# Kernel tuning notes

Hardware: AMD Instinct MI355X
Metric: run time of the kernel (lower is better)

Reference implementation:

```python
import jax, jax.numpy as jnp
import numpy as np

BS, D_IN, D_H, D_Z = 4096, 784, 400, 20


def setup_inputs() -> dict:
    key = jax.random.key(0)
    ks = jax.random.split(key, 13)
    s = 0.05
    return {
        "x": jax.random.normal(ks[0], (BS, D_IN), dtype=jnp.float32),
        "W1": jax.random.normal(ks[1], (D_H, D_IN), dtype=jnp.float32) * s,
        "b1": jax.random.normal(ks[2], (D_H,), dtype=jnp.float32) * s,
        "W21": jax.random.normal(ks[3], (D_Z, D_H), dtype=jnp.float32) * s,
        "b21": jax.random.normal(ks[4], (D_Z,), dtype=jnp.float32) * s,
        "W22": jax.random.normal(ks[5], (D_Z, D_H), dtype=jnp.float32) * s,
        "b22": jax.random.normal(ks[6], (D_Z,), dtype=jnp.float32) * s,
        "W3": jax.random.normal(ks[7], (D_H, D_Z), dtype=jnp.float32) * s,
        "b3": jax.random.normal(ks[8], (D_H,), dtype=jnp.float32) * s,
        "W41": jax.random.normal(ks[9], (D_IN, D_H), dtype=jnp.float32) * s,
        "b41": jax.random.normal(ks[10], (D_IN,), dtype=jnp.float32) * s,
        "W42": jax.random.normal(ks[11], (D_IN, D_H), dtype=jnp.float32) * s,
        "b42": jax.random.normal(ks[12], (D_IN,), dtype=jnp.float32) * s,
    }


def reference(x, W1, b1, W21, b21, W22, b22, W3, b3, W41, b41, W42, b42):
    xr = x.reshape(-1, D_IN)                              # [bs, 784]
    # encode
    h1 = jax.nn.relu(xr @ W1.T + b1)                      # [bs, 400]
    mu = h1 @ W21.T + b21                                 # [bs, 20]
    logvar = h1 @ W22.T + b22                             # [bs, 20]
    # unscented sigma points: varsqrt[:, i] = sqrt(N)*logvar[:, i]*e_i
    N = D_Z
    sqrtN = jnp.asarray(np.sqrt(N), dtype=x.dtype)
    # delta[i, b, j] = sqrt(N) * logvar[b, i] * (i == j)   -> [N, bs, N]
    delta = sqrtN * logvar.T[:, :, None] * jnp.eye(N, dtype=x.dtype)[:, None, :]
    z = jnp.concatenate([mu[None] + delta, mu[None] - delta], axis=0)  # [2N, bs, N]

    def decode(zs):
        h3 = jax.nn.relu(zs @ W3.T + b3)                  # [bs, 400]
        return zs @ W41.T * 0 + (h3 @ W41.T + b41), h3 @ W42.T + b42

    def decode_clean(zs):
        h3 = jax.nn.relu(zs @ W3.T + b3)
        return h3 @ W41.T + b41, h3 @ W42.T + b42

    # original loop decodes every sigma point; recon_x keeps the last one
    mu_x, var_x = jax.vmap(decode_clean)(z)               # each [2N, bs, 784]
    recon_mu = mu_x[-1]
    recon_var = var_x[-1]
    return recon_mu, recon_var, mu, logvar, z
```

## Files before the change

kernel.cpp:

```cpp
#include <hip/hip_runtime.h>
#include <hip/hip_bf16.h>

#define BS   4096
#define DIN  784
#define DH   400
#define DZ   20

#define KPH  416
#define KPD  448

#define OFF_RMU  0
#define OFF_RVAR 3211264
#define OFF_MU   6422528
#define OFF_LV   6504448
#define OFF_Z    6586368

#define WS_WCAT  0
#define WS_W2C   1404928
#define WS_H1B   1444864
#define WS_H3B   4852736

#define SQRT20F 4.47213595499958f

using short8 = __attribute__((ext_vector_type(8))) short;
using f4     = __attribute__((ext_vector_type(4))) float;

__device__ __forceinline__ short bf16r(float f) {
    union { float f; unsigned u; } v; v.f = f;
    unsigned r = (v.u + 0x7fffu + ((v.u >> 16) & 1u)) >> 16;
    return (short)r;
}

__device__ __forceinline__ void glds16(const void* g, void* l) {
    __builtin_amdgcn_global_load_lds(
        (const __attribute__((address_space(1))) unsigned int*)g,
        (__attribute__((address_space(3))) unsigned int*)l,
        16, 0, 0);
}

__global__ __launch_bounds__(256)
void k1(const float* __restrict__ x, const float* __restrict__ W1,
        const float* __restrict__ b1,
        const float* __restrict__ W41, const float* __restrict__ W42,
        const float* __restrict__ W21, const float* __restrict__ W22,
        short* __restrict__ h1b, char* __restrict__ ws) {
    __shared__ short sA[2][64 * 64];
    __shared__ short sB[2][80 * 64];

    const int tid = threadIdx.x;
    const int bid = blockIdx.x;

    if (bid >= 320) {
        short* wcat = (short*)(ws + WS_WCAT);
        short* w2c  = (short*)(ws + WS_W2C);
        const int NC = 1568 * 56 + 48 * 52;
        for (int p = (bid - 320) * 256 + tid; p < NC; p += 64 * 256) {
            const float* sr = nullptr;
            short* dst;
            int c;
            if (p < 1568 * 56) {
                int row = p / 56; c = p - row * 56;
                sr = (row < 784) ? (W41 + (size_t)row * DH)
                                 : (W42 + (size_t)(row - 784) * DH);
                dst = wcat + (size_t)row * KPD + c * 8;
            } else {
                int q = p - 1568 * 56;
                int row = q / 52; c = q - row * 52;
                if (row < 20)      sr = W21 + (size_t)row * DH;
                else if (row < 40) sr = W22 + (size_t)(row - 20) * DH;
                dst = w2c + (size_t)row * KPH + c * 8;
            }
            short8 v;
            if (c < 50 && sr) {
                f4 a = *(const f4*)(sr + c * 8);
                f4 b = *(const f4*)(sr + c * 8 + 4);
#pragma unroll
                for (int e = 0; e < 4; ++e) { v[e] = bf16r(a[e]); v[4 + e] = bf16r(b[e]); }
            } else {
#pragma unroll
                for (int e = 0; e < 8; ++e) v[e] = 0;
            }
            *(short8*)dst = v;
        }
        return;
    }

    const int swz = (bid & 7) * 40 + (bid >> 3);
    const int bm = swz / 5, bn = swz - bm * 5;
    const int w = tid >> 6, l = tid & 63, lg = l >> 4, lr = l & 15;

    f4 acc[5] = {};
    f4 ar[4];
    f4 br[6];

    auto a_load = [&](int kt) {
#pragma unroll
        for (int i = 0; i < 2; ++i) {
            int c = tid + i * 256;
            int row = c >> 3, kc = c & 7;
            int gk = kt * 64 + kc * 8;
            if (gk < DIN) {
                const float* src = x + (size_t)(bm * 64 + row) * DIN + gk;
                ar[2 * i] = *(const f4*)src;
                ar[2 * i + 1] = *(const f4*)(src + 4);
            } else {
                ar[2 * i] = (f4){0.f, 0.f, 0.f, 0.f};
                ar[2 * i + 1] = (f4){0.f, 0.f, 0.f, 0.f};
            }
        }
    };
    auto b_load = [&](int kt) {
#pragma unroll
        for (int i = 0; i < 3; ++i) {
            int c = tid + i * 256;
            if (c < 640) {
                int row = c >> 3, kc = c & 7;
                int gk = kt * 64 + kc * 8;
                if (gk < DIN) {
                    const float* src = W1 + (size_t)(bn * 80 + row) * DIN + gk;
                    br[2 * i] = *(const f4*)src;
                    br[2 * i + 1] = *(const f4*)(src + 4);
                } else {
                    br[2 * i] = (f4){0.f, 0.f, 0.f, 0.f};
                    br[2 * i + 1] = (f4){0.f, 0.f, 0.f, 0.f};
                }
            }
        }
    };
    auto ab_write = [&](int buf) {
#pragma unroll
        for (int i = 0; i < 2; ++i) {
            int c = tid + i * 256;
            int row = c >> 3, kc = c & 7;
            short8 v;
#pragma unroll
            for (int e = 0; e < 4; ++e) { v[e] = bf16r(ar[2 * i][e]); v[4 + e] = bf16r(ar[2 * i + 1][e]); }
            *(short8*)&sA[buf][(row * 8 + (kc ^ (row & 7))) * 8] = v;
        }
#pragma unroll
        for (int i = 0; i < 3; ++i) {
            int c = tid + i * 256;
            if (c < 640) {
                int row = c >> 3, kc = c & 7;
                short8 v;
#pragma unroll
                for (int e = 0; e < 4; ++e) { v[e] = bf16r(br[2 * i][e]); v[4 + e] = bf16r(br[2 * i + 1][e]); }
                *(short8*)&sB[buf][(row * 8 + (kc ^ (row & 7))) * 8] = v;
            }
        }
    };
    auto compute = [&](int buf) {
        const int row = w * 16 + lr;
#pragma unroll
        for (int kk = 0; kk < 2; ++kk) {
            short8 a = *(const short8*)&sA[buf][(row * 8 + ((kk * 4 + lg) ^ (row & 7))) * 8];
#pragma unroll
            for (int ni = 0; ni < 5; ++ni) {
                int brw = ni * 16 + lr;
                short8 b = *(const short8*)&sB[buf][(brw * 8 + ((kk * 4 + lg) ^ (brw & 7))) * 8];
                acc[ni] = __builtin_amdgcn_mfma_f32_16x16x32_bf16(a, b, acc[ni], 0, 0, 0);
            }
        }
    };

    a_load(0); b_load(0); ab_write(0);
    __syncthreads();
    for (int kt = 0; kt < 13; ++kt) {
        const int cur = kt & 1;
        if (kt < 12) { a_load(kt + 1); b_load(kt + 1); }
        compute(cur);
        if (kt < 12) ab_write(cur ^ 1);
        __syncthreads();
    }

#pragma unroll
    for (int ni = 0; ni < 5; ++ni) {
        int col = bn * 80 + ni * 16 + lr;
        float bias = b1[col];
#pragma unroll
        for (int r = 0; r < 4; ++r) {
            int row = bm * 64 + w * 16 + lg * 4 + r;
            float v = acc[ni][r] + bias;
            h1b[(size_t)row * KPH + col] = bf16r(v > 0.f ? v : 0.f);
        }
    }
    if (bn == 4) {
        for (int p = tid; p < 64 * 16; p += 256) {
            int r = p >> 4, c = 400 + (p & 15);
            h1b[(size_t)(bm * 64 + r) * KPH + c] = 0;
        }
    }
}

__global__ __launch_bounds__(256)
void k_mid(const short* __restrict__ h1b, const short* __restrict__ w2c,
           const float* __restrict__ W3, const float* __restrict__ b3,
           const float* __restrict__ b21, const float* __restrict__ b22,
           float* __restrict__ out, short* __restrict__ h3b) {
    __shared__ short sA[16 * 416];
    __shared__ short sB[48 * 416];
    __shared__ short sW[400 * 40];
    __shared__ float muv[2][16][20];
    __shared__ short zl[16 * 40];
    __shared__ short h3s[16 * 448];

    const int tid = threadIdx.x;
    const int blk = blockIdx.x;
    const int w = tid >> 6, l = tid & 63, lg = l >> 4, lr = l & 15;
    const int r0 = blk * 16;

#pragma unroll
    for (int it = 0; it < 4; ++it) {
        int p = it * 256 + tid;
        if (p < 832) {
            int r = p / 52, cp = p - r * 52, c = cp ^ (r & 3);
            glds16(h1b + (size_t)(r0 + r) * KPH + c * 8, &sA[p * 8]);
        }
    }
#pragma unroll
    for (int it = 0; it < 10; ++it) {
        int p = it * 256 + tid;
        if (p < 2496) {
            int r = p / 52, cp = p - r * 52, c = cp ^ (r & 3);
            glds16(w2c + (size_t)r * KPH + c * 8, &sB[p * 8]);
        }
    }
    if (tid < 200) {
#pragma unroll
        for (int i = 0; i < 2; ++i) {
            int r = tid + i * 200;
            const float* src = W3 + (size_t)r * DZ;
            f4 f0 = *(const f4*)src;
            f4 f1 = *(const f4*)(src + 4);
            f4 f2 = *(const f4*)(src + 8);
            f4 f3 = *(const f4*)(src + 12);
            f4 f5 = *(const f4*)(src + 16);
            short8 c0, c1, c2, c3;
#pragma unroll
            for (int e = 0; e < 4; ++e) {
                c0[e] = bf16r(f0[e]); c0[4 + e] = bf16r(f1[e]);
                c1[e] = bf16r(f2[e]); c1[4 + e] = bf16r(f3[e]);
                c2[e] = bf16r(f5[e]); c2[4 + e] = 0;
                c3[e] = 0; c3[4 + e] = 0;
            }
            *(short8*)&sW[r * 40 + 0]  = c0;
            *(short8*)&sW[r * 40 + 8]  = c1;
            *(short8*)&sW[r * 40 + 16] = c2;
            *(short8*)&sW[r * 40 + 24] = c3;
        }
    }
    __syncthreads();

    if (w == 0) {
        f4 a3[3] = {};
#pragma unroll
        for (int kk = 0; kk < 13; ++kk) {
            short8 a = *(const short8*)&sA[(lr * 52 + ((kk * 4 + lg) ^ (lr & 3))) * 8];
#pragma unroll
            for (int ni = 0; ni < 3; ++ni) {
                int br = ni * 16 + lr;
                short8 b = *(const short8*)&sB[(br * 52 + ((kk * 4 + lg) ^ (br & 3))) * 8];
                a3[ni] = __builtin_amdgcn_mfma_f32_16x16x32_bf16(a, b, a3[ni], 0, 0, 0);
            }
        }
#pragma unroll
        for (int ni = 0; ni < 3; ++ni) {
            int n = ni * 16 + lr;
            if (n < 40) {
                float bias = (n < 20) ? b21[n] : b22[n - 20];
#pragma unroll
                for (int r = 0; r < 4; ++r) {
                    int row = lg * 4 + r;
                    float v = a3[ni][r] + bias;
                    if (n < 20) {
                        muv[0][row][n] = v;
                        out[OFF_MU + (size_t)(r0 + row) * 20 + n] = v;
                    } else {
                        muv[1][row][n - 20] = v;
                        out[OFF_LV + (size_t)(r0 + row) * 20 + (n - 20)] = v;
                    }
                }
            }
        }
    }
    __syncthreads();

    if (tid < 80) {
        int row = tid / 5, c = tid - (tid / 5) * 5;
        short8 v;
#pragma unroll
        for (int e = 0; e < 8; ++e) {
            int j = c * 8 + e;
            float val = 0.f;
            if (j < 20) {
                val = muv[0][row][j];
                if (j == 19) val -= SQRT20F * muv[1][row][19];
            }
            v[e] = bf16r(val);
        }
        *(short8*)&zl[row * 40 + c * 8] = v;
    } else if (tid < 176) {
        int t = tid - 80;
        int row = t / 6, c = t - (t / 6) * 6;
        short8 zz;
#pragma unroll
        for (int e = 0; e < 8; ++e) zz[e] = 0;
        *(short8*)&h3s[row * 448 + 400 + c * 8] = zz;
    }
#pragma unroll
    for (int it = 0; it < 13; ++it) {
        int p = it * 256 + tid;
        if (p < 3200) {
            int s = p / 80, q = p - s * 80;
            int row = q / 5, j4 = q - (q / 5) * 5;
            f4 v = *(const f4*)&muv[0][row][j4 * 4];
            int sp = (s < 20) ? s : s - 20;
            if ((sp >> 2) == j4) {
                float add = ((s < 20) ? SQRT20F : -SQRT20F) * muv[1][row][sp];
                int e = sp & 3;
#pragma unroll
                for (int k = 0; k < 4; ++k) v[k] += (e == k) ? add : 0.f;
            }
            *(f4*)(out + OFF_Z + ((size_t)s * BS + r0 + row) * 20 + j4 * 4) = v;
        }
    }
    __syncthreads();

    for (int f = w; f < 25; f += 4) {
        int n0 = f * 16;
        short8 a = *(const short8*)&zl[lr * 40 + lg * 8];
        short8 b = *(const short8*)&sW[(n0 + lr) * 40 + lg * 8];
        f4 z4 = {};
        f4 accv = __builtin_amdgcn_mfma_f32_16x16x32_bf16(a, b, z4, 0, 0, 0);
        int n = n0 + lr;
        float bias = b3[n];
#pragma unroll
        for (int r = 0; r < 4; ++r) {
            int row = lg * 4 + r;
            float v = accv[r] + bias;
            h3s[row * 448 + n] = bf16r(v > 0.f ? v : 0.f);
        }
    }
    __syncthreads();

#pragma unroll
    for (int it = 0; it < 4; ++it) {
        int p = it * 256 + tid;
        if (p < 896) {
            int row = p / 56, c = p - (p / 56) * 56;
            *(short8*)(h3b + (size_t)(r0 + row) * KPD + c * 8) =
                *(const short8*)&h3s[row * 448 + c * 8];
        }
    }
}

__global__ __launch_bounds__(256)
void k_gemm4(const short* __restrict__ h3b, const short* __restrict__ wcat,
             const float* __restrict__ b41, const float* __restrict__ b42,
             float* __restrict__ out) {
    __shared__ short sA[2][64 * 64];
    __shared__ short sB[2][112 * 64];

    const int tid = threadIdx.x;
    const int bid = blockIdx.x;
    const int swz = (bid & 7) * 112 + (bid >> 3);
    const int bm = swz / 14, bn = swz - bm * 14;
    const int w = tid >> 6, l = tid & 63, lg = l >> 4, lr = l & 15;

    f4 acc[7] = {};

    auto stage = [&](int buf, int kt) {
#pragma unroll
        for (int i = 0; i < 2; ++i) {
            int c = tid + i * 256;
            int r = c >> 3, kc = (c & 7) ^ (r & 7);
            glds16(h3b + (size_t)(bm * 64 + r) * KPD + kt * 64 + kc * 8, &sA[buf][c * 8]);
        }
#pragma unroll
        for (int i = 0; i < 4; ++i) {
            int c = tid + i * 256;
            if (c < 896) {
                int r = c >> 3, kc = (c & 7) ^ (r & 7);
                glds16(wcat + (size_t)(bn * 112 + r) * KPD + kt * 64 + kc * 8, &sB[buf][c * 8]);
            }
        }
    };

    stage(0, 0);
    __syncthreads();
    for (int kt = 0; kt < 7; ++kt) {
        const int cur = kt & 1;
        if (kt < 6) stage(cur ^ 1, kt + 1);
        const int arow = w * 16 + lr;
#pragma unroll
        for (int kk = 0; kk < 2; ++kk) {
            short8 a = *(const short8*)&sA[cur][(arow * 8 + ((kk * 4 + lg) ^ (arow & 7))) * 8];
#pragma unroll
            for (int ni = 0; ni < 7; ++ni) {
                int br = ni * 16 + lr;
                short8 b = *(const short8*)&sB[cur][(br * 8 + ((kk * 4 + lg) ^ (br & 7))) * 8];
                acc[ni] = __builtin_amdgcn_mfma_f32_16x16x32_bf16(a, b, acc[ni], 0, 0, 0);
            }
        }
        __syncthreads();
    }

    const bool first = (bn < 7);
#pragma unroll
    for (int ni = 0; ni < 7; ++ni) {
        int colt = bn * 112 + ni * 16 + lr;
        int cc = first ? colt : colt - 784;
        float bias = first ? b41[cc] : b42[cc];
        size_t base = first ? (size_t)OFF_RMU : (size_t)OFF_RVAR;
#pragma unroll
        for (int r = 0; r < 4; ++r) {
            size_t row = (size_t)(bm * 64 + w * 16 + lg * 4 + r);
            out[base + row * DIN + cc] = acc[ni][r] + bias;
        }
    }
}

extern "C" void kernel_launch(void* const* d_in, const int* in_sizes, int n_in,
                              void* d_out, int out_size, void* d_ws, size_t ws_size,
                              hipStream_t stream) {
    const float* x   = (const float*)d_in[0];
    const float* W1  = (const float*)d_in[1];
    const float* b1  = (const float*)d_in[2];
    const float* W21 = (const float*)d_in[3];
    const float* b21 = (const float*)d_in[4];
    const float* W22 = (const float*)d_in[5];
    const float* b22 = (const float*)d_in[6];
    const float* W3  = (const float*)d_in[7];
    const float* b3  = (const float*)d_in[8];
    const float* W41 = (const float*)d_in[9];
    const float* b41 = (const float*)d_in[10];
    const float* W42 = (const float*)d_in[11];
    const float* b42 = (const float*)d_in[12];

    float* out = (float*)d_out;
    char*  ws  = (char*)d_ws;
    const short* wcat = (const short*)(ws + WS_WCAT);
    const short* w2c  = (const short*)(ws + WS_W2C);
    short* h1b = (short*)(ws + WS_H1B);
    short* h3b = (short*)(ws + WS_H3B);

    k1<<<384, 256, 0, stream>>>(x, W1, b1, W41, W42, W21, W22, h1b, ws);
    k_mid<<<256, 256, 0, stream>>>(h1b, w2c, W3, b3, b21, b22, out, h3b);
    k_gemm4<<<896, 256, 0, stream>>>(h3b, wcat, b41, b42, out);
}
```

Measured before the change: 49.11 us.

## Deepen k1 prefetch, truncate bf16 packing, enlarge gemm4 tiles, move z writes

In k1, fp32-to-bf16 conversion becomes truncation: each pair of floats is packed by taking their high halves. The single-stage register prefetch becomes a two-set, distance-two prefetch with explicit barriers. In k_gemm4, the M tile grows from 64 to 128 rows so each B tile is reused twice, which halves the GEMM block count. The z sigma-point output writes move out of k_mid into 64 extra blocks of k_gemm4 that read mu and logvar back from the output buffer. Truncation instead of round-to-nearest changes numerics slightly, and the larger tile means fewer blocks and more registers per thread.

```diff
diff --git a/kernel.cpp b/kernel.cpp
--- a/kernel.cpp
+++ b/kernel.cpp
@@ -24,11 +24,21 @@
 
 using short8 = __attribute__((ext_vector_type(8))) short;
 using f4     = __attribute__((ext_vector_type(4))) float;
+using i4     = __attribute__((ext_vector_type(4))) int;
 
 __device__ __forceinline__ short bf16r(float f) {
     union { float f; unsigned u; } v; v.f = f;
     unsigned r = (v.u + 0x7fffu + ((v.u >> 16) & 1u)) >> 16;
     return (short)r;
+}
+
+__device__ __forceinline__ i4 pack8(const i4 q0, const i4 q1) {
+    i4 d;
+    d[0] = (q0[1] & 0xffff0000) | (int)(((unsigned)q0[0]) >> 16);
+    d[1] = (q0[3] & 0xffff0000) | (int)(((unsigned)q0[2]) >> 16);
+    d[2] = (q1[1] & 0xffff0000) | (int)(((unsigned)q1[0]) >> 16);
+    d[3] = (q1[3] & 0xffff0000) | (int)(((unsigned)q1[2]) >> 16);
+    return d;
 }
 
 __device__ __forceinline__ void glds16(const void* g, void* l) {
@@ -90,26 +100,21 @@
     const int w = tid >> 6, l = tid & 63, lg = l >> 4, lr = l & 15;
 
     f4 acc[5] = {};
-    f4 ar[4];
-    f4 br[6];
-
-    auto a_load = [&](int kt) {
+    i4 A0[4], A1[4], B0[6], B1[6];
+
+    auto loadT = [&](int kt, i4* qa, i4* qb) {
 #pragma unroll
         for (int i = 0; i < 2; ++i) {
             int c = tid + i * 256;
             int row = c >> 3, kc = c & 7;
             int gk = kt * 64 + kc * 8;
             if (gk < DIN) {
-                const float* src = x + (size_t)(bm * 64 + row) * DIN + gk;
-                ar[2 * i] = *(const f4*)src;
-                ar[2 * i + 1] = *(const f4*)(src + 4);
+                const i4* p = (const i4*)(x + (size_t)(bm * 64 + row) * DIN + gk);
+                qa[2 * i] = p[0]; qa[2 * i + 1] = p[1];
             } else {
-                ar[2 * i] = (f4){0.f, 0.f, 0.f, 0.f};
-                ar[2 * i + 1] = (f4){0.f, 0.f, 0.f, 0.f};
-            }
-        }
-    };
-    auto b_load = [&](int kt) {
+                qa[2 * i] = (i4){0, 0, 0, 0}; qa[2 * i + 1] = (i4){0, 0, 0, 0};
+            }
+        }
 #pragma unroll
         for (int i = 0; i < 3; ++i) {
             int c = tid + i * 256;
@@ -117,35 +122,27 @@
                 int row = c >> 3, kc = c & 7;
                 int gk = kt * 64 + kc * 8;
                 if (gk < DIN) {
-                    const float* src = W1 + (size_t)(bn * 80 + row) * DIN + gk;
-                    br[2 * i] = *(const f4*)src;
-                    br[2 * i + 1] = *(const f4*)(src + 4);
+                    const i4* p = (const i4*)(W1 + (size_t)(bn * 80 + row) * DIN + gk);
+                    qb[2 * i] = p[0]; qb[2 * i + 1] = p[1];
                 } else {
-                    br[2 * i] = (f4){0.f, 0.f, 0.f, 0.f};
-                    br[2 * i + 1] = (f4){0.f, 0.f, 0.f, 0.f};
+                    qb[2 * i] = (i4){0, 0, 0, 0}; qb[2 * i + 1] = (i4){0, 0, 0, 0};
                 }
             }
         }
     };
-    auto ab_write = [&](int buf) {
+    auto writeT = [&](int buf, const i4* qa, const i4* qb) {
 #pragma unroll
         for (int i = 0; i < 2; ++i) {
             int c = tid + i * 256;
             int row = c >> 3, kc = c & 7;
-            short8 v;
-#pragma unroll
-            for (int e = 0; e < 4; ++e) { v[e] = bf16r(ar[2 * i][e]); v[4 + e] = bf16r(ar[2 * i + 1][e]); }
-            *(short8*)&sA[buf][(row * 8 + (kc ^ (row & 7))) * 8] = v;
+            *(i4*)&sA[buf][(row * 8 + (kc ^ (row & 7))) * 8] = pack8(qa[2 * i], qa[2 * i + 1]);
         }
 #pragma unroll
         for (int i = 0; i < 3; ++i) {
             int c = tid + i * 256;
             if (c < 640) {
                 int row = c >> 3, kc = c & 7;
-                short8 v;
-#pragma unroll
-                for (int e = 0; e < 4; ++e) { v[e] = bf16r(br[2 * i][e]); v[4 + e] = bf16r(br[2 * i + 1][e]); }
-                *(short8*)&sB[buf][(row * 8 + (kc ^ (row & 7))) * 8] = v;
+                *(i4*)&sB[buf][(row * 8 + (kc ^ (row & 7))) * 8] = pack8(qb[2 * i], qb[2 * i + 1]);
             }
         }
     };
@@ -163,14 +160,37 @@
         }
     };
 
-    a_load(0); b_load(0); ab_write(0);
-    __syncthreads();
-    for (int kt = 0; kt < 13; ++kt) {
-        const int cur = kt & 1;
-        if (kt < 12) { a_load(kt + 1); b_load(kt + 1); }
-        compute(cur);
-        if (kt < 12) ab_write(cur ^ 1);
-        __syncthreads();
+    loadT(0, A0, B0);
+    writeT(0, A0, B0);
+    loadT(1, A1, B1);
+    loadT(2, A0, B0);
+    asm volatile("s_waitcnt lgkmcnt(0)" ::: "memory");
+    __builtin_amdgcn_sched_barrier(0);
+    __builtin_amdgcn_s_barrier();
+    __builtin_amdgcn_sched_barrier(0);
+
+#pragma unroll
+    for (int kt2 = 0; kt2 < 13; kt2 += 2) {
+        {
+            const int kt = kt2;
+            compute(0);
+            if (kt <= 11) writeT(1, A1, B1);
+            if (kt <= 9)  loadT(kt + 3, A1, B1);
+            asm volatile("s_waitcnt lgkmcnt(0)" ::: "memory");
+            __builtin_amdgcn_sched_barrier(0);
+            __builtin_amdgcn_s_barrier();
+            __builtin_amdgcn_sched_barrier(0);
+        }
+        if (kt2 + 1 < 13) {
+            const int kt = kt2 + 1;
+            compute(1);
+            if (kt <= 11) writeT(0, A0, B0);
+            if (kt <= 9)  loadT(kt + 3, A0, B0);
+            asm volatile("s_waitcnt lgkmcnt(0)" ::: "memory");
+            __builtin_amdgcn_sched_barrier(0);
+            __builtin_amdgcn_s_barrier();
+            __builtin_amdgcn_sched_barrier(0);
+        }
     }
 
 #pragma unroll
@@ -307,23 +327,6 @@
         for (int e = 0; e < 8; ++e) zz[e] = 0;
         *(short8*)&h3s[row * 448 + 400 + c * 8] = zz;
     }
-#pragma unroll
-    for (int it = 0; it < 13; ++it) {
-        int p = it * 256 + tid;
-        if (p < 3200) {
-            int s = p / 80, q = p - s * 80;
-            int row = q / 5, j4 = q - (q / 5) * 5;
-            f4 v = *(const f4*)&muv[0][row][j4 * 4];
-            int sp = (s < 20) ? s : s - 20;
-            if ((sp >> 2) == j4) {
-                float add = ((s < 20) ? SQRT20F : -SQRT20F) * muv[1][row][sp];
-                int e = sp & 3;
-#pragma unroll
-                for (int k = 0; k < 4; ++k) v[k] += (e == k) ? add : 0.f;
-            }
-            *(f4*)(out + OFF_Z + ((size_t)s * BS + r0 + row) * 20 + j4 * 4) = v;
-        }
-    }
     __syncthreads();
 
     for (int f = w; f < 25; f += 4) {
@@ -358,23 +361,45 @@
 void k_gemm4(const short* __restrict__ h3b, const short* __restrict__ wcat,
              const float* __restrict__ b41, const float* __restrict__ b42,
              float* __restrict__ out) {
-    __shared__ short sA[2][64 * 64];
+    __shared__ short sA[2][128 * 64];
     __shared__ short sB[2][112 * 64];
 
     const int tid = threadIdx.x;
     const int bid = blockIdx.x;
-    const int swz = (bid & 7) * 112 + (bid >> 3);
+
+    if (bid >= 448) {
+        const int zb = bid - 448;
+#pragma unroll 2
+        for (int it = 0; it < 50; ++it) {
+            int idx = it * 16384 + zb * 256 + tid;
+            int s = idx / 20480;
+            int rem = idx - s * 20480;
+            int b = rem / 5, j4 = rem - b * 5;
+            int sp = (s < 20) ? s : s - 20;
+            f4 v = *(const f4*)(out + OFF_MU + (size_t)b * 20 + j4 * 4);
+            if ((sp >> 2) == j4) {
+                float add = ((s < 20) ? SQRT20F : -SQRT20F) * out[OFF_LV + (size_t)b * 20 + sp];
+                int e = sp & 3;
+#pragma unroll
+                for (int k = 0; k < 4; ++k) v[k] += (e == k) ? add : 0.f;
+            }
+            *(f4*)(out + OFF_Z + (size_t)idx * 4) = v;
+        }
+        return;
+    }
+
+    const int swz = (bid & 7) * 56 + (bid >> 3);
     const int bm = swz / 14, bn = swz - bm * 14;
     const int w = tid >> 6, l = tid & 63, lg = l >> 4, lr = l & 15;
 
-    f4 acc[7] = {};
+    f4 acc[2][7] = {};
 
     auto stage = [&](int buf, int kt) {
 #pragma unroll
-        for (int i = 0; i < 2; ++i) {
+        for (int i = 0; i < 4; ++i) {
             int c = tid + i * 256;
             int r = c >> 3, kc = (c & 7) ^ (r & 7);
-            glds16(h3b + (size_t)(bm * 64 + r) * KPD + kt * 64 + kc * 8, &sA[buf][c * 8]);
+            glds16(h3b + (size_t)(bm * 128 + r) * KPD + kt * 64 + kc * 8, &sA[buf][c * 8]);
         }
 #pragma unroll
         for (int i = 0; i < 4; ++i) {
@@ -391,15 +416,17 @@
     for (int kt = 0; kt < 7; ++kt) {
         const int cur = kt & 1;
         if (kt < 6) stage(cur ^ 1, kt + 1);
-        const int arow = w * 16 + lr;
+        const int row0 = w * 32 + lr, row1 = w * 32 + 16 + lr;
 #pragma unroll
         for (int kk = 0; kk < 2; ++kk) {
-            short8 a = *(const short8*)&sA[cur][(arow * 8 + ((kk * 4 + lg) ^ (arow & 7))) * 8];
+            short8 a0 = *(const short8*)&sA[cur][(row0 * 8 + ((kk * 4 + lg) ^ (row0 & 7))) * 8];
+            short8 a1 = *(const short8*)&sA[cur][(row1 * 8 + ((kk * 4 + lg) ^ (row1 & 7))) * 8];
 #pragma unroll
             for (int ni = 0; ni < 7; ++ni) {
                 int br = ni * 16 + lr;
                 short8 b = *(const short8*)&sB[cur][(br * 8 + ((kk * 4 + lg) ^ (br & 7))) * 8];
-                acc[ni] = __builtin_amdgcn_mfma_f32_16x16x32_bf16(a, b, acc[ni], 0, 0, 0);
+                acc[0][ni] = __builtin_amdgcn_mfma_f32_16x16x32_bf16(a0, b, acc[0][ni], 0, 0, 0);
+                acc[1][ni] = __builtin_amdgcn_mfma_f32_16x16x32_bf16(a1, b, acc[1][ni], 0, 0, 0);
             }
         }
         __syncthreads();
@@ -407,17 +434,19 @@
 
     const bool first = (bn < 7);
 #pragma unroll
-    for (int ni = 0; ni < 7; ++ni) {
-        int colt = bn * 112 + ni * 16 + lr;
-        int cc = first ? colt : colt - 784;
-        float bias = first ? b41[cc] : b42[cc];
-        size_t base = first ? (size_t)OFF_RMU : (size_t)OFF_RVAR;
-#pragma unroll
-        for (int r = 0; r < 4; ++r) {
-            size_t row = (size_t)(bm * 64 + w * 16 + lg * 4 + r);
-            out[base + row * DIN + cc] = acc[ni][r] + bias;
-        }
-    }
+    for (int mi = 0; mi < 2; ++mi)
+#pragma unroll
+        for (int ni = 0; ni < 7; ++ni) {
+            int colt = bn * 112 + ni * 16 + lr;
+            int cc = first ? colt : colt - 784;
+            float bias = first ? b41[cc] : b42[cc];
+            size_t base = first ? (size_t)OFF_RMU : (size_t)OFF_RVAR;
+#pragma unroll
+            for (int r = 0; r < 4; ++r) {
+                size_t row = (size_t)(bm * 128 + w * 32 + mi * 16 + lg * 4 + r);
+                out[base + row * DIN + cc] = acc[mi][ni][r] + bias;
+            }
+        }
 }
 
 extern "C" void kernel_launch(void* const* d_in, const int* in_sizes, int n_in,
@@ -446,5 +475,5 @@
 
     k1<<<384, 256, 0, stream>>>(x, W1, b1, W41, W42, W21, W22, h1b, ws);
     k_mid<<<256, 256, 0, stream>>>(h1b, w2c, W3, b3, b21, b22, out, h3b);
-    k_gemm4<<<896, 256, 0, stream>>>(h3b, wcat, b41, b42, out);
-}
+    k_gemm4<<<512, 256, 0, stream>>>(h3b, wcat, b41, b42, out);
+}
```

Measured after the change: 49.89 us. About the same (+1.6%).
